# Kernel tuning notes

Hardware: AMD Instinct MI355X
Metric: run time of the kernel (lower is better)

Reference implementation:

```python
import jax, jax.numpy as jnp
import numpy as np

B, T, C, H = 2, 2048, 1024, 16
HD = C // H            # 64
LAYER_IDX, N_LAYER = 5, 12
BASE = 16
# window_mode='power_2.0': progress=(5+1)/12=0.5; window=max(16, int(16+0.5**2*(2048-16)))=524
WINDOW = max(BASE, int(BASE + ((LAYER_IDX + 1) / N_LAYER) ** 2.0 * (T - BASE)))
WINDOW = min(WINDOW, T)


def setup_inputs() -> dict:
    key = jax.random.key(0)
    ks = jax.random.split(key, 6)
    x = jax.random.normal(ks[0], (B, T, C), dtype=jnp.float32)
    Wq = jax.random.normal(ks[1], (C, C), dtype=jnp.float32) * 0.02
    Wk = jax.random.normal(ks[2], (C, C), dtype=jnp.float32) * 0.02
    Wv = jax.random.normal(ks[3], (C, C), dtype=jnp.float32) * 0.02
    Wo = jax.random.normal(ks[4], (C, C), dtype=jnp.float32) * 0.02
    # RoPE tables: angles theta_i = t / 10000^(i/(HD/2)), shape (T,1,HD//2) to broadcast over (B,T,H,HD//2)
    half = HD // 2
    inv_freq = 1.0 / (10000.0 ** (jnp.arange(half, dtype=jnp.float32) / half))
    ang = jnp.arange(T, dtype=jnp.float32)[:, None] * inv_freq[None, :]  # (T, half)
    rope_cos = jnp.cos(ang)[:, None, :]  # (T,1,half)
    rope_sin = jnp.sin(ang)[:, None, :]
    return {"x": x, "Wq": Wq, "Wk": Wk, "Wv": Wv, "Wo": Wo,
            "rope_cos": rope_cos, "rope_sin": rope_sin}


def _apply_rotary(x, cos, sin):
    d = x.shape[-1] // 2
    x1, x2 = x[..., :d], x[..., d:]
    return jnp.concatenate([x1 * cos + x2 * sin, -x2 * sin + x1 * cos], axis=-1)


def reference(x, Wq, Wk, Wv, Wo, rope_cos, rope_sin):
    Bv, Tv, Cv = x.shape
    q = (x @ Wq).reshape(Bv, Tv, H, HD)
    k = (x @ Wk).reshape(Bv, Tv, H, HD)
    v = (x @ Wv).reshape(Bv, Tv, H, HD)
    q = _apply_rotary(q, rope_cos, rope_sin)
    k = _apply_rotary(k, rope_cos, rope_sin)
    # sliding-window causal mask: cols<=rows and cols>=rows-WINDOW+1
    rows = jnp.arange(Tv)[:, None]
    cols = jnp.arange(Tv)[None, :]
    allowed = (cols <= rows) & (cols >= rows - WINDOW + 1)  # (T,T)
    scale = 1.0 / np.sqrt(HD)
    scores = jnp.einsum('bthd,bshd->bhts', q, k) * scale  # (B,H,T,T)
    scores = jnp.where(allowed[None, None], scores, -jnp.inf)
    attn = jax.nn.softmax(scores, axis=-1)
    y = jnp.einsum('bhts,bshd->bthd', attn, v).reshape(Bv, Tv, Cv)
    return y @ Wo
```

## Files before the change

kernel.cpp:

```cpp
#include <hip/hip_runtime.h>
#include <math.h>

typedef unsigned short u16;
typedef unsigned int u32;
typedef __bf16 bf16x8 __attribute__((ext_vector_type(8)));
typedef float f32x4 __attribute__((ext_vector_type(4)));
typedef unsigned short ushort4v __attribute__((ext_vector_type(4)));

#define T_SEQ 2048
#define WIN_M1 523
#define QSCALE 0.180336879f
#define MASKV -1e30f

__device__ __forceinline__ u16 f2b(float f) {
  union { float f; unsigned int u; } v; v.f = f;
  unsigned int u = v.u;
  u += 0x7FFFu + ((u >> 16) & 1u);
  return (u16)(u >> 16);
}

__device__ __forceinline__ u32 cvtpk(float lo, float hi) {
  union { __bf16 h[2]; u32 d; } cv;
  cv.h[0] = (__bf16)lo;
  cv.h[1] = (__bf16)hi;
  return cv.d;
}

__device__ __forceinline__ float fexp2(float x) {
  return __builtin_amdgcn_exp2f(x);
}

__device__ __forceinline__ void load_lds16(const u16* g, u16* l) {
  __builtin_amdgcn_global_load_lds(
      (const __attribute__((address_space(1))) void*)g,
      (__attribute__((address_space(3))) void*)l, 16, 0, 0);
}

__global__ void prep_k(const float* __restrict__ x, u16* __restrict__ xb,
                       const float* __restrict__ W0, const float* __restrict__ W1,
                       const float* __restrict__ W2, const float* __restrict__ W3,
                       u16* __restrict__ WcatT, u16* __restrict__ WoT) {
  const int bid = blockIdx.x;
  if (bid < 4096) {
    int i = bid * 256 + threadIdx.x;
    float4 v = ((const float4*)x)[i];
    u16* d = xb + i * 4;
    d[0] = f2b(v.x); d[1] = f2b(v.y); d[2] = f2b(v.z); d[3] = f2b(v.w);
    return;
  }
  __shared__ float tile[32][33];
  const int t = bid - 4096;
  const int z = t >> 10, i = t & 1023;
  const float* W = (z == 0) ? W0 : (z == 1) ? W1 : (z == 2) ? W2 : W3;
  u16* Wt = (z < 3) ? (WcatT + (size_t)z * 1024 * 1024) : WoT;
  int tx = threadIdx.x & 31, ty = threadIdx.x >> 5;
  int n0 = (i & 31) * 32, k0 = (i >> 5) * 32;
#pragma unroll
  for (int j = 0; j < 4; ++j)
    tile[ty + j * 8][tx] = W[(size_t)(k0 + ty + j * 8) * 1024 + n0 + tx];
  __syncthreads();
#pragma unroll
  for (int j = 0; j < 4; ++j)
    Wt[(size_t)(n0 + ty + j * 8) * 1024 + k0 + tx] = f2b(tile[tx][ty + j * 8]);
}

template <int MODE>
__global__ __launch_bounds__(256, 4) void gemm_k(
    const u16* __restrict__ A, const u16* __restrict__ Bt,
    float* __restrict__ outf,
    u16* __restrict__ Qo, u16* __restrict__ Ko, u16* __restrict__ Vto,
    const float* __restrict__ rc, const float* __restrict__ rs) {
  __shared__ alignas(16) u16 As[3][128 * 32];
  __shared__ alignas(16) u16 Bs[3][128 * 32];
  const int tid = threadIdx.x, lane = tid & 63, w = tid >> 6;
  const int l15 = lane & 15, q4 = lane >> 4;
  const int row0 = blockIdx.y * 128, col0 = blockIdx.x * 128;
  const int wm = w >> 1, wn = w & 1;
  constexpr int NT = 32;

  f32x4 acc[4][4];
#pragma unroll
  for (int i = 0; i < 4; ++i)
#pragma unroll
    for (int j = 0; j < 4; ++j) acc[i][j] = (f32x4){0.f, 0.f, 0.f, 0.f};

  const int off0 = (w * 2) * 1024 + lane * 16;
  const int r0 = off0 >> 6, c0 = (off0 & 63) >> 1;
  const int off1 = off0 + 1024;
  const int r1 = off1 >> 6, c1 = (off1 & 63) >> 1;
  const u16* gA0 = A + (size_t)(row0 + r0) * 1024 + c0;
  const u16* gA1 = A + (size_t)(row0 + r1) * 1024 + c1;
  const u16* gB0 = Bt + (size_t)(col0 + r0) * 1024 + c0;
  const u16* gB1 = Bt + (size_t)(col0 + r1) * 1024 + c1;
  const int soff = (w * 2) * 512;

  auto stage = [&](int buf, int t) {
    const int k0 = t * 32;
    load_lds16(gA0 + k0, &As[buf][soff]);
    load_lds16(gA1 + k0, &As[buf][soff + 512]);
    load_lds16(gB0 + k0, &Bs[buf][soff]);
    load_lds16(gB1 + k0, &Bs[buf][soff + 512]);
  };
  auto compute = [&](int buf) {
    bf16x8 af[4], bfr[4];
#pragma unroll
    for (int im = 0; im < 4; ++im)
      af[im] = *(const bf16x8*)&As[buf][(wm * 64 + im * 16 + l15) * 32 + q4 * 8];
#pragma unroll
    for (int jn = 0; jn < 4; ++jn)
      bfr[jn] = *(const bf16x8*)&Bs[buf][(wn * 64 + jn * 16 + l15) * 32 + q4 * 8];
#pragma unroll
    for (int im = 0; im < 4; ++im)
#pragma unroll
      for (int jn = 0; jn < 4; ++jn)
        acc[im][jn] = __builtin_amdgcn_mfma_f32_16x16x32_bf16(af[im], bfr[jn], acc[im][jn], 0, 0, 0);
  };

  stage(0, 0);
  stage(1, 1);
  int bs = 2, bc = 0;
  for (int t = 0; t + 2 < NT; ++t) {
    stage(bs, t + 2);
    asm volatile("s_waitcnt vmcnt(8)" ::: "memory");
    __builtin_amdgcn_s_barrier();
    compute(bc);
    __builtin_amdgcn_s_barrier();
    bs = (bs + 1 == 3) ? 0 : bs + 1;
    bc = (bc + 1 == 3) ? 0 : bc + 1;
  }
  asm volatile("s_waitcnt vmcnt(4)" ::: "memory");
  __builtin_amdgcn_s_barrier();
  compute(bc);
  __builtin_amdgcn_s_barrier();
  bc = (bc + 1 == 3) ? 0 : bc + 1;
  asm volatile("s_waitcnt vmcnt(0)" ::: "memory");
  __builtin_amdgcn_s_barrier();
  compute(bc);

  if constexpr (MODE == 0) {
#pragma unroll
    for (int im = 0; im < 4; ++im) {
      const int rowb = row0 + wm * 64 + im * 16 + q4 * 4;
      const int b = rowb >> 11, t0 = rowb & 2047;
#pragma unroll
      for (int jn = 0; jn < 2; ++jn) {
        const int n = col0 + wn * 64 + jn * 16 + l15;
        const int sel = n >> 10, nn = n & 1023;
        const int h = nn >> 6, hd = nn & 63;
        if (sel < 2) {
          const float qs = (sel == 0) ? QSCALE : 1.0f;
          u16* dst = (sel == 0 ? Qo : Ko) + ((size_t)(b * 16 + h) * 2048) * 64;
#pragma unroll
          for (int r = 0; r < 4; ++r) {
            const int tt = t0 + r;
            const float c = rc[tt * 32 + hd], s = rs[tt * 32 + hd];
            const float x1 = acc[im][jn][r], x2 = acc[im][jn + 2][r];
            dst[(size_t)tt * 64 + hd] = f2b((x1 * c + x2 * s) * qs);
            dst[(size_t)tt * 64 + hd + 32] = f2b((x1 * c - x2 * s) * qs);
          }
        } else {
          ushort4v p1, p2;
#pragma unroll
          for (int r = 0; r < 4; ++r) {
            p1[r] = f2b(acc[im][jn][r]);
            p2[r] = f2b(acc[im][jn + 2][r]);
          }
          u16* dst = Vto + (size_t)(b * 16 + h) * 64 * 2048 + t0;
          *(ushort4v*)(dst + (size_t)hd * 2048) = p1;
          *(ushort4v*)(dst + (size_t)(hd + 32) * 2048) = p2;
        }
      }
    }
  } else {
#pragma unroll
    for (int im = 0; im < 4; ++im) {
      const int rowb = row0 + wm * 64 + im * 16 + q4 * 4;
#pragma unroll
      for (int jn = 0; jn < 4; ++jn) {
        const int n = col0 + wn * 64 + jn * 16 + l15;
#pragma unroll
        for (int r = 0; r < 4; ++r)
          outf[(size_t)(rowb + r) * 1024 + n] = acc[im][jn][r];
      }
    }
  }
}

__global__ __launch_bounds__(256) void attn_k(
    const u16* __restrict__ Q, const u16* __restrict__ Kk,
    const u16* __restrict__ Vt, u16* __restrict__ Y) {
  const int lane = threadIdx.x & 63, w = threadIdx.x >> 6;
  const int l15 = lane & 15, q4 = lane >> 4;
  const int hw = blockIdx.x;
  const int work = (hw & 7) * 64 + (hw >> 3);
  const int bh = work >> 4;
  const int qt = 15 - (work & 15);
  const int q0 = qt * 128 + w * 32;
  const u16* Qb = Q + (size_t)bh * 2048 * 64;
  const u16* Kb = Kk + (size_t)bh * 2048 * 64;
  const u16* Vb = Vt + (size_t)bh * 64 * 2048;

  bf16x8 bq[2][2];
#pragma unroll
  for (int qs = 0; qs < 2; ++qs)
#pragma unroll
    for (int kb = 0; kb < 2; ++kb)
      bq[qs][kb] = *(const bf16x8*)(Qb + (size_t)(q0 + qs * 16 + l15) * 64 + kb * 32 + q4 * 8);

  f32x4 o[2][4];
#pragma unroll
  for (int qs = 0; qs < 2; ++qs)
#pragma unroll
    for (int jo = 0; jo < 4; ++jo) o[qs][jo] = (f32x4){0.f, 0.f, 0.f, 0.f};
  float lp[2] = {0.f, 0.f};

  int s0 = q0 - WIN_M1; if (s0 < 0) s0 = 0; s0 &= ~31;
  const int srcA = l15 + ((q4 & 1) << 5);
  const int srcB = srcA + 16;
  const bool lowq4 = (q4 < 2);

  bf16x8 kc[2][2], kn[2][2];
  bf16x8 vc[4], vn[4];
#pragma unroll
  for (int ks = 0; ks < 2; ++ks)
#pragma unroll
    for (int kb = 0; kb < 2; ++kb)
      kc[ks][kb] = *(const bf16x8*)(Kb + (size_t)(s0 + ks * 16 + l15) * 64 + kb * 32 + q4 * 8);
#pragma unroll
  for (int jo = 0; jo < 4; ++jo)
    vc[jo] = *(const bf16x8*)(Vb + (size_t)(jo * 16 + l15) * 2048 + s0 + q4 * 8);

  int kv0 = s0;

#define TILE_BODY(KC, VC, KN, VN)                                                      \
  {                                                                                    \
    const int kvn = kv0 + 32;                                                          \
    if (kvn <= q0) {                                                                   \
      _Pragma("unroll") for (int ks = 0; ks < 2; ++ks)                                 \
          _Pragma("unroll") for (int kb = 0; kb < 2; ++kb)                             \
              KN[ks][kb] = *(const bf16x8*)(Kb + (size_t)(kvn + ks * 16 + l15) * 64 +  \
                                            kb * 32 + q4 * 8);                         \
      _Pragma("unroll") for (int jo = 0; jo < 4; ++jo)                                 \
          VN[jo] = *(const bf16x8*)(Vb + (size_t)(jo * 16 + l15) * 2048 + kvn +        \
                                    q4 * 8);                                           \
    }                                                                                  \
    f32x4 ss[2][2];                                                                    \
    _Pragma("unroll") for (int ks = 0; ks < 2; ++ks)                                   \
        _Pragma("unroll") for (int qs = 0; qs < 2; ++qs)                               \
            ss[ks][qs] = (f32x4){0.f, 0.f, 0.f, 0.f};                                  \
    _Pragma("unroll") for (int kb = 0; kb < 2; ++kb)                                   \
        _Pragma("unroll") for (int ks = 0; ks < 2; ++ks)                               \
            _Pragma("unroll") for (int qs = 0; qs < 2; ++qs)                           \
                ss[ks][qs] = __builtin_amdgcn_mfma_f32_16x16x32_bf16(                  \
                    KC[ks][kb], bq[qs][kb], ss[ks][qs], 0, 0, 0);                      \
    if ((kv0 + 32 > q0) || (kv0 < q0 - 492)) {                                         \
      _Pragma("unroll") for (int qs = 0; qs < 2; ++qs) {                               \
        const int tq = q0 + qs * 16 + l15;                                             \
        _Pragma("unroll") for (int ks = 0; ks < 2; ++ks)                               \
            _Pragma("unroll") for (int r = 0; r < 4; ++r) {                            \
          const int kv = kv0 + ks * 16 + q4 * 4 + r;                                   \
          if (kv > tq || kv < tq - WIN_M1) ss[ks][qs][r] = MASKV;                      \
        }                                                                              \
      }                                                                                \
    }                                                                                  \
    _Pragma("unroll") for (int qs = 0; qs < 2; ++qs) {                                 \
      float p[2][4];                                                                   \
      _Pragma("unroll") for (int ks = 0; ks < 2; ++ks)                                 \
          _Pragma("unroll") for (int r = 0; r < 4; ++r)                                \
              p[ks][r] = fexp2(ss[ks][qs][r]);                                         \
      lp[qs] += ((p[0][0] + p[0][1]) + (p[0][2] + p[0][3])) +                          \
                ((p[1][0] + p[1][1]) + (p[1][2] + p[1][3]));                           \
      const u32 a0 = cvtpk(p[0][0], p[0][1]), a1 = cvtpk(p[0][2], p[0][3]);            \
      const u32 b0 = cvtpk(p[1][0], p[1][1]), b1 = cvtpk(p[1][2], p[1][3]);            \
      union { u32 d[4]; bf16x8 v; } pu;                                                \
      const u32 d0a = (u32)__shfl((int)a0, srcA), d0b = (u32)__shfl((int)b0, srcA);    \
      const u32 d1a = (u32)__shfl((int)a1, srcA), d1b = (u32)__shfl((int)b1, srcA);    \
      const u32 d2a = (u32)__shfl((int)a0, srcB), d2b = (u32)__shfl((int)b0, srcB);    \
      const u32 d3a = (u32)__shfl((int)a1, srcB), d3b = (u32)__shfl((int)b1, srcB);    \
      pu.d[0] = lowq4 ? d0a : d0b;                                                     \
      pu.d[1] = lowq4 ? d1a : d1b;                                                     \
      pu.d[2] = lowq4 ? d2a : d2b;                                                     \
      pu.d[3] = lowq4 ? d3a : d3b;                                                     \
      _Pragma("unroll") for (int jo = 0; jo < 4; ++jo)                                 \
          o[qs][jo] = __builtin_amdgcn_mfma_f32_16x16x32_bf16(pu.v, VC[jo],            \
                                                              o[qs][jo], 0, 0, 0);     \
    }                                                                                  \
  }

  while (true) {
    TILE_BODY(kc, vc, kn, vn);
    kv0 += 32; if (kv0 > q0) break;
    TILE_BODY(kn, vn, kc, vc);
    kv0 += 32; if (kv0 > q0) break;
  }
#undef TILE_BODY

  const int b = bh >> 4, h = bh & 15;
  u16* Yb = Y + (size_t)(b * 2048 + q0) * 1024 + h * 64 + l15;
#pragma unroll
  for (int qs = 0; qs < 2; ++qs) {
    float l = lp[qs];
    l += __shfl_xor(l, 16);
    l += __shfl_xor(l, 32);
#pragma unroll
    for (int r = 0; r < 4; ++r) {
      const float lv = __shfl(l, q4 * 4 + r);
      const float inv = 1.0f / lv;
      u16* yr = Yb + (size_t)(qs * 16 + q4 * 4 + r) * 1024;
#pragma unroll
      for (int jo = 0; jo < 4; ++jo) yr[jo * 16] = f2b(o[qs][jo][r] * inv);
    }
  }
}

extern "C" void kernel_launch(void* const* d_in, const int* in_sizes, int n_in,
                              void* d_out, int out_size, void* d_ws, size_t ws_size,
                              hipStream_t stream) {
  const float* x = (const float*)d_in[0];
  const float* Wq = (const float*)d_in[1];
  const float* Wk = (const float*)d_in[2];
  const float* Wv = (const float*)d_in[3];
  const float* Wo = (const float*)d_in[4];
  const float* rc = (const float*)d_in[5];
  const float* rs = (const float*)d_in[6];
  float* out = (float*)d_out;
  char* ws = (char*)d_ws;
  const size_t MB = 1024 * 1024;
  u16* xb = (u16*)(ws);
  u16* WcatT = (u16*)(ws + 8 * MB);
  u16* WoT = (u16*)(ws + 14 * MB);
  u16* Qr = (u16*)(ws + 16 * MB);
  u16* Kr = (u16*)(ws + 24 * MB);
  u16* Vt = (u16*)(ws + 32 * MB);
  u16* Y = (u16*)(ws + 40 * MB);

  prep_k<<<8192, 256, 0, stream>>>(x, xb, Wq, Wk, Wv, Wo, WcatT, WoT);
  gemm_k<0><<<dim3(24, 32), 256, 0, stream>>>(xb, WcatT, nullptr, Qr, Kr, Vt, rc, rs);
  attn_k<<<512, 256, 0, stream>>>(Qr, Kr, Vt, Y);
  gemm_k<1><<<dim3(8, 32), 256, 0, stream>>>(Y, WoT, out, nullptr, nullptr, nullptr, nullptr, nullptr);
}
```

Before: 108.7 us.

## Store Q, K, V in MFMA fragment-order tiles for contiguous attention loads

The QKV GEMM epilogue now writes Q, K and transposed V into blocked layouts where each 16x32 (or 16x32 for V) MFMA operand fragment is stored as one contiguous 1KB chunk indexed by lane. The attention kernel then loads each fragment with a single fully coalesced lane*8 access instead of strided row accesses. The cost is that the GEMM epilogue stores become more scattered (scalar u16 writes to permuted addresses), which may hurt the producer kernel.

```diff
diff --git a/kernel.cpp b/kernel.cpp
--- a/kernel.cpp
+++ b/kernel.cpp
@@ -35,6 +35,7 @@
       (const __attribute__((address_space(1))) void*)g,
       (__attribute__((address_space(3))) void*)l, 16, 0, 0);
 }
+
 
 __global__ void prep_k(const float* __restrict__ x, u16* __restrict__ xb,
                        const float* __restrict__ W0, const float* __restrict__ W1,
@@ -147,27 +148,38 @@
         const int n = col0 + wn * 64 + jn * 16 + l15;
         const int sel = n >> 10, nn = n & 1023;
         const int h = nn >> 6, hd = nn & 63;
+        const int bhi = b * 16 + h;
         if (sel < 2) {
           const float qs = (sel == 0) ? QSCALE : 1.0f;
-          u16* dst = (sel == 0 ? Qo : Ko) + ((size_t)(b * 16 + h) * 2048) * 64;
+          u16* base = (sel == 0 ? Qo : Ko);
+          const int q4c = (hd >> 3) & 3, e = hd & 7;
 #pragma unroll
           for (int r = 0; r < 4; ++r) {
             const int tt = t0 + r;
             const float c = rc[tt * 32 + hd], s = rs[tt * 32 + hd];
             const float x1 = acc[im][jn][r], x2 = acc[im][jn + 2][r];
-            dst[(size_t)tt * 64 + hd] = f2b((x1 * c + x2 * s) * qs);
-            dst[(size_t)tt * 64 + hd + 32] = f2b((x1 * c - x2 * s) * qs);
+            const size_t blk = ((size_t)bhi * 128 + (tt >> 4)) * 2;
+            const size_t off = (size_t)q4c * 128 + (size_t)(tt & 15) * 8 + e;
+            base[(blk << 9) + off] = f2b((x1 * c + x2 * s) * qs);
+            base[((blk + 1) << 9) + off] = f2b((x1 * c - x2 * s) * qs);
           }
         } else {
+          const int kv32 = t0 >> 5;
+          const int q4w = (t0 >> 3) & 3;
+          const int e0 = t0 & 7;
+          const int jo1 = hd >> 4;
+          const int l15r = hd & 15;
           ushort4v p1, p2;
 #pragma unroll
           for (int r = 0; r < 4; ++r) {
             p1[r] = f2b(acc[im][jn][r]);
             p2[r] = f2b(acc[im][jn + 2][r]);
           }
-          u16* dst = Vto + (size_t)(b * 16 + h) * 64 * 2048 + t0;
-          *(ushort4v*)(dst + (size_t)hd * 2048) = p1;
-          *(ushort4v*)(dst + (size_t)(hd + 32) * 2048) = p2;
+          const size_t off = (size_t)q4w * 128 + (size_t)l15r * 8 + e0;
+          const size_t b1 = ((((size_t)bhi * 64 + kv32) * 4 + jo1) << 9) + off;
+          const size_t b2 = ((((size_t)bhi * 64 + kv32) * 4 + jo1 + 2) << 9) + off;
+          *(ushort4v*)(Vto + b1) = p1;
+          *(ushort4v*)(Vto + b2) = p2;
         }
       }
     }
@@ -196,16 +208,15 @@
   const int bh = work >> 4;
   const int qt = 15 - (work & 15);
   const int q0 = qt * 128 + w * 32;
-  const u16* Qb = Q + (size_t)bh * 2048 * 64;
-  const u16* Kb = Kk + (size_t)bh * 2048 * 64;
-  const u16* Vb = Vt + (size_t)bh * 64 * 2048;
+
+  const int qt16 = q0 >> 4;
 
   bf16x8 bq[2][2];
 #pragma unroll
   for (int qs = 0; qs < 2; ++qs)
 #pragma unroll
     for (int kb = 0; kb < 2; ++kb)
-      bq[qs][kb] = *(const bf16x8*)(Qb + (size_t)(q0 + qs * 16 + l15) * 64 + kb * 32 + q4 * 8);
+      bq[qs][kb] = *(const bf16x8*)(Q + ((((size_t)bh * 128 + qt16 + qs) * 2 + kb) << 9) + lane * 8);
 
   f32x4 o[2][4];
 #pragma unroll
@@ -225,10 +236,10 @@
   for (int ks = 0; ks < 2; ++ks)
 #pragma unroll
     for (int kb = 0; kb < 2; ++kb)
-      kc[ks][kb] = *(const bf16x8*)(Kb + (size_t)(s0 + ks * 16 + l15) * 64 + kb * 32 + q4 * 8);
+      kc[ks][kb] = *(const bf16x8*)(Kk + ((((size_t)bh * 128 + (s0 >> 4) + ks) * 2 + kb) << 9) + lane * 8);
 #pragma unroll
   for (int jo = 0; jo < 4; ++jo)
-    vc[jo] = *(const bf16x8*)(Vb + (size_t)(jo * 16 + l15) * 2048 + s0 + q4 * 8);
+    vc[jo] = *(const bf16x8*)(Vt + ((((size_t)bh * 64 + (s0 >> 5)) * 4 + jo) << 9) + lane * 8);
 
   int kv0 = s0;
 
@@ -238,11 +249,11 @@
     if (kvn <= q0) {                                                                   \
       _Pragma("unroll") for (int ks = 0; ks < 2; ++ks)                                 \
           _Pragma("unroll") for (int kb = 0; kb < 2; ++kb)                             \
-              KN[ks][kb] = *(const bf16x8*)(Kb + (size_t)(kvn + ks * 16 + l15) * 64 +  \
-                                            kb * 32 + q4 * 8);                         \
+              KN[ks][kb] = *(const bf16x8*)(Kk +                                       \
+                  ((((size_t)bh * 128 + (kvn >> 4) + ks) * 2 + kb) << 9) + lane * 8);  \
       _Pragma("unroll") for (int jo = 0; jo < 4; ++jo)                                 \
-          VN[jo] = *(const bf16x8*)(Vb + (size_t)(jo * 16 + l15) * 2048 + kvn +        \
-                                    q4 * 8);                                           \
+          VN[jo] = *(const bf16x8*)(Vt +                                               \
+              ((((size_t)bh * 64 + (kvn >> 5)) * 4 + jo) << 9) + lane * 8);            \
     }                                                                                  \
     f32x4 ss[2][2];                                                                    \
     _Pragma("unroll") for (int ks = 0; ks < 2; ++ks)                                   \
@@ -329,13 +340,13 @@
   u16* xb = (u16*)(ws);
   u16* WcatT = (u16*)(ws + 8 * MB);
   u16* WoT = (u16*)(ws + 14 * MB);
-  u16* Qr = (u16*)(ws + 16 * MB);
-  u16* Kr = (u16*)(ws + 24 * MB);
-  u16* Vt = (u16*)(ws + 32 * MB);
+  u16* Qf = (u16*)(ws + 16 * MB);
+  u16* Kf = (u16*)(ws + 24 * MB);
+  u16* Vf = (u16*)(ws + 32 * MB);
   u16* Y = (u16*)(ws + 40 * MB);
 
   prep_k<<<8192, 256, 0, stream>>>(x, xb, Wq, Wk, Wv, Wo, WcatT, WoT);
-  gemm_k<0><<<dim3(24, 32), 256, 0, stream>>>(xb, WcatT, nullptr, Qr, Kr, Vt, rc, rs);
-  attn_k<<<512, 256, 0, stream>>>(Qr, Kr, Vt, Y);
+  gemm_k<0><<<dim3(24, 32), 256, 0, stream>>>(xb, WcatT, nullptr, Qf, Kf, Vf, rc, rs);
+  attn_k<<<512, 256, 0, stream>>>(Qf, Kf, Vf, Y);
   gemm_k<1><<<dim3(8, 32), 256, 0, stream>>>(Y, WoT, out, nullptr, nullptr, nullptr, nullptr, nullptr);
 }
```

Measured after the change: 95.08 us. 1.14x faster.
